# Kernel tuning notes

Hardware: AMD Instinct MI355X
Metric: run time of the kernel (lower is better)

The kernel has to match this reference:

```python
import jax, jax.numpy as jnp
import numpy as np

B, T, C = 2, 2048, 2048
N_HEAD, N_KV = 16, 4
HD = C // N_HEAD          # 128
ROPE_THETA = 10000.0


def setup_inputs() -> dict:
    key = jax.random.key(0)
    ks = jax.random.split(key, 6)
    std = 0.02
    x = jax.random.normal(ks[0], (B, T, C), dtype=jnp.float32)
    Wq = jax.random.normal(ks[1], (C, C), dtype=jnp.float32) * std
    Wk = jax.random.normal(ks[2], (C, N_KV * HD), dtype=jnp.float32) * std
    Wv = jax.random.normal(ks[3], (C, N_KV * HD), dtype=jnp.float32) * std
    Wo = jax.random.normal(ks[4], (C, C), dtype=jnp.float32) * std
    # real RoPE frequencies: freqs_cis = exp(i * t * theta^{-2j/hd})
    inv_freq = 1.0 / (ROPE_THETA ** (jnp.arange(0, HD, 2, dtype=jnp.float32) / HD))
    ang = jnp.arange(T, dtype=jnp.float32)[:, None] * inv_freq[None, :]  # [T, HD//2]
    return {"x": x, "Wq": Wq, "Wk": Wk, "Wv": Wv, "Wo": Wo,
            "freqs_cos": jnp.cos(ang), "freqs_sin": jnp.sin(ang)}


def _rope(t, cos, sin):
    # t: [B, H, T, HD]; cos/sin: [T, HD//2] -> complex rotate even/odd pairs
    tr = t.reshape(*t.shape[:-1], HD // 2, 2)
    re, im = tr[..., 0], tr[..., 1]
    c = cos[None, None, :, :]
    s = sin[None, None, :, :]
    out = jnp.stack([re * c - im * s, re * s + im * c], axis=-1)
    return out.reshape(t.shape)


def reference(x, Wq, Wk, Wv, Wo, freqs_cos, freqs_sin):
    Bm, Tm, Cm = x.shape
    q = (x @ Wq).reshape(Bm, Tm, N_HEAD, HD).transpose(0, 2, 1, 3)  # [B,H,T,HD]
    k = (x @ Wk).reshape(Bm, Tm, N_KV, HD).transpose(0, 2, 1, 3)    # [B,Hkv,T,HD]
    v = (x @ Wv).reshape(Bm, Tm, N_KV, HD).transpose(0, 2, 1, 3)
    q = _rope(q, freqs_cos, freqs_sin)
    k = _rope(k, freqs_cos, freqs_sin)
    rep = N_HEAD // N_KV
    k = jnp.repeat(k, rep, axis=1)  # GQA repeat_kv -> [B,H,T,HD]
    v = jnp.repeat(v, rep, axis=1)
    scale = 1.0 / jnp.sqrt(jnp.asarray(HD, dtype=x.dtype))
    att = jnp.einsum("bhqd,bhkd->bhqk", q, k) * scale
    causal = jnp.tril(jnp.ones((Tm, Tm), dtype=bool))
    att = jnp.where(causal[None, None], att, jnp.asarray(-jnp.inf, att.dtype))
    att = jax.nn.softmax(att, axis=-1)
    y = jnp.einsum("bhqk,bhkd->bhqd", att, v)
    y = y.transpose(0, 2, 1, 3).reshape(Bm, Tm, Cm)
    return y @ Wo
```

## Files before the change

### kernel.cpp

```cpp
#include <hip/hip_runtime.h>

#define B_ 2
#define T_ 2048
#define C_ 2048
#define NH_ 16
#define NKV_ 4
#define HD_ 128
#define REP_ (NH_ / NKV_)
#define LDQKV 3072

typedef unsigned short u16;
typedef __bf16 bf16x8v __attribute__((ext_vector_type(8)));
typedef float f32x4v __attribute__((ext_vector_type(4)));

__device__ __forceinline__ u16 f2bf(float f) {
    unsigned int u;
    __builtin_memcpy(&u, &f, 4);
    u += 0x7FFFu + ((u >> 16) & 1u);
    return (u16)(u >> 16);
}
__device__ __forceinline__ unsigned int pk2(float a, float b) {
    unsigned int ua, ub;
    __builtin_memcpy(&ua, &a, 4);
    __builtin_memcpy(&ub, &b, 4);
    ua += 0x8000u; ub += 0x8000u;
    return (ua >> 16) | (ub & 0xFFFF0000u);
}
__device__ __forceinline__ bf16x8v load8(const u16* p) {
    return *reinterpret_cast<const bf16x8v*>(p);
}
__device__ __forceinline__ void gl16(const u16* g, u16* l) {
    __builtin_amdgcn_global_load_lds(
        (const __attribute__((address_space(1))) void*)(g),
        (__attribute__((address_space(3))) void*)(l), 16, 0, 0);
}

__global__ void cvt_f32_bf16(const float* __restrict__ in, u16* __restrict__ out, int n4) {
    int i = blockIdx.x * blockDim.x + threadIdx.x;
    if (i >= n4) return;
    float4 v = reinterpret_cast<const float4*>(in)[i];
    ushort4 o;
    o.x = f2bf(v.x); o.y = f2bf(v.y); o.z = f2bf(v.z); o.w = f2bf(v.w);
    reinterpret_cast<ushort4*>(out)[i] = o;
}

__global__ void xpose_f32_bf16(const float* __restrict__ in, u16* __restrict__ out,
                               int R, int Cc) {
    __shared__ u16 tile[32][33];
    int bx = blockIdx.x * 32, by = blockIdx.y * 32;
    int tx = threadIdx.x, ty = threadIdx.y;
    for (int i = 0; i < 32; i += 8)
        tile[ty + i][tx] = f2bf(in[(size_t)(by + ty + i) * Cc + bx + tx]);
    __syncthreads();
    for (int i = 0; i < 32; i += 8)
        out[(size_t)(bx + ty + i) * R + by + tx] = tile[tx][ty + i];
}

__global__ __launch_bounds__(256) void gemm_qkv(const u16* __restrict__ A,
                                                const u16* __restrict__ BT,
                                                u16* __restrict__ Cq,
                                                u16* __restrict__ vtb,
                                                int M, int N, int K) {
    __shared__ __align__(16) u16 As[128 * 32];
    __shared__ __align__(16) u16 Bs[128 * 32];
    int tid = threadIdx.x;
    int lane = tid & 63, wave = tid >> 6;
    int wm = wave & 1, wn = wave >> 1;
    int row = lane & 15, quad = lane >> 4;
    int m0 = blockIdx.y * 128, n0 = blockIdx.x * 128;

    int r_ = tid >> 2, c_ = tid & 3;
    int gch = c_ ^ ((r_ >> 1) & 3);
    const u16* gA = A + (size_t)(m0 + r_) * K + gch * 8;
    const u16* gB = BT + (size_t)(n0 + r_) * K + gch * 8;
    u16* lA = As + tid * 8;
    u16* lB = Bs + tid * 8;

    int swf = (quad ^ ((row >> 1) & 3)) * 8;
    const u16* a0 = As + (wm * 64 + row) * 32 + swf;
    const u16* b0 = Bs + (wn * 64 + row) * 32 + swf;

    f32x4v acc[4][4] = {};
    for (int k0 = 0; k0 < K; k0 += 32) {
        __syncthreads();
        gl16(gA, lA); gl16(gA + (size_t)64 * K, lA + 2048);
        gl16(gB, lB); gl16(gB + (size_t)64 * K, lB + 2048);
        gA += 32; gB += 32;
        __syncthreads();
        bf16x8v af[4], bfv[4];
        for (int t = 0; t < 4; t++) {
            af[t] = load8(a0 + t * 512);
            bfv[t] = load8(b0 + t * 512);
        }
        for (int mt = 0; mt < 4; mt++)
            for (int nt = 0; nt < 4; nt++)
                acc[mt][nt] = __builtin_amdgcn_mfma_f32_16x16x32_bf16(
                    af[mt], bfv[nt], acc[mt][nt], 0, 0, 0);
    }

    if (n0 >= 2560) {
        for (int mt = 0; mt < 4; mt++)
            for (int nt = 0; nt < 4; nt++) {
                int hd = n0 + wn * 64 + nt * 16 + row - 2560;
                int mbase = m0 + wm * 64 + mt * 16 + quad * 4;
                int bb = mbase >> 11, tok = mbase & 2047;
                int g = (tok & 31) >> 2;
                int off = (tok & ~31) + ((g & 3) * 8 + (g >> 2) * 4);
                ushort4 pk;
                pk.x = f2bf(acc[mt][nt][0]);
                pk.y = f2bf(acc[mt][nt][1]);
                pk.z = f2bf(acc[mt][nt][2]);
                pk.w = f2bf(acc[mt][nt][3]);
                *reinterpret_cast<ushort4*>(vtb + ((size_t)bb * 512 + hd) * T_ + off) = pk;
            }
    } else {
        for (int mt = 0; mt < 4; mt++)
            for (int nt = 0; nt < 4; nt++) {
                int c = n0 + wn * 64 + nt * 16 + row;
                for (int r = 0; r < 4; r++) {
                    int mrow = m0 + wm * 64 + mt * 16 + quad * 4 + r;
                    Cq[(size_t)mrow * N + c] = f2bf(acc[mt][nt][r]);
                }
            }
    }
}

__global__ __launch_bounds__(256) void gemm_out(const u16* __restrict__ A,
                                                const u16* __restrict__ BT,
                                                float* __restrict__ C,
                                                int M, int N, int K) {
    __shared__ __align__(16) u16 As[128 * 32];
    __shared__ __align__(16) u16 Bs[128 * 32];
    int tid = threadIdx.x;
    int lane = tid & 63, wave = tid >> 6;
    int wm = wave & 1, wn = wave >> 1;
    int row = lane & 15, quad = lane >> 4;
    int m0 = blockIdx.y * 128, n0 = blockIdx.x * 128;

    int r_ = tid >> 2, c_ = tid & 3;
    int gch = c_ ^ ((r_ >> 1) & 3);
    const u16* gA = A + (size_t)(m0 + r_) * K + gch * 8;
    const u16* gB = BT + (size_t)(n0 + r_) * K + gch * 8;
    u16* lA = As + tid * 8;
    u16* lB = Bs + tid * 8;

    int swf = (quad ^ ((row >> 1) & 3)) * 8;
    const u16* a0 = As + (wm * 64 + row) * 32 + swf;
    const u16* b0 = Bs + (wn * 64 + row) * 32 + swf;

    f32x4v acc[4][4] = {};
    for (int k0 = 0; k0 < K; k0 += 32) {
        __syncthreads();
        gl16(gA, lA); gl16(gA + (size_t)64 * K, lA + 2048);
        gl16(gB, lB); gl16(gB + (size_t)64 * K, lB + 2048);
        gA += 32; gB += 32;
        __syncthreads();
        bf16x8v af[4], bfv[4];
        for (int t = 0; t < 4; t++) {
            af[t] = load8(a0 + t * 512);
            bfv[t] = load8(b0 + t * 512);
        }
        for (int mt = 0; mt < 4; mt++)
            for (int nt = 0; nt < 4; nt++)
                acc[mt][nt] = __builtin_amdgcn_mfma_f32_16x16x32_bf16(
                    af[mt], bfv[nt], acc[mt][nt], 0, 0, 0);
    }

    for (int mt = 0; mt < 4; mt++)
        for (int nt = 0; nt < 4; nt++) {
            int c = n0 + wn * 64 + nt * 16 + row;
            for (int r = 0; r < 4; r++) {
                int mrow = m0 + wm * 64 + mt * 16 + quad * 4 + r;
                C[(size_t)mrow * N + c] = acc[mt][nt][r];
            }
        }
}

__global__ void rope_fused(u16* __restrict__ qkvb, const float* __restrict__ cb,
                           const float* __restrict__ sb, int totq) {
    int idx = blockIdx.x * blockDim.x + threadIdx.x;
    int nheads, off;
    if (idx < totq) { nheads = NH_; off = 0; }
    else { idx -= totq; nheads = NKV_; off = 2048; }
    int i = idx & 63;
    int h = (idx >> 6) % nheads;
    int bt = idx / (64 * nheads);
    int tt = bt & (T_ - 1);
    u16* p = qkvb + (size_t)bt * LDQKV + off + h * HD_ + 2 * i;
    unsigned int ure = ((unsigned int)p[0]) << 16, uim = ((unsigned int)p[1]) << 16;
    float re, im;
    __builtin_memcpy(&re, &ure, 4);
    __builtin_memcpy(&im, &uim, 4);
    float c = cb[tt * 64 + i], s = sb[tt * 64 + i];
    p[0] = f2bf(re * c - im * s);
    p[1] = f2bf(re * s + im * c);
}

__device__ __forceinline__ void stage_k128(const u16* kB, u16* Kl, int kt, int tid) {
    int keyc = tid >> 4, ch = tid & 15;
    const u16* g = kB + (size_t)(kt + keyc) * LDQKV + (ch ^ keyc) * 8;
    u16* l = Kl + tid * 8;
    for (int j = 0; j < 8; j++) {
        gl16(g, l);
        g += (size_t)16 * LDQKV;
        l += 2048;
    }
}
__device__ __forceinline__ void stage_v128(const u16* vB, u16* Vl, int kt, int tid) {
    int hdc = tid >> 4, ch = tid & 15;
    const u16* g = vB + (size_t)hdc * T_ + kt + (ch ^ hdc) * 8;
    u16* l = Vl + tid * 8;
    for (int j = 0; j < 8; j++) {
        gl16(g, l);
        g += (size_t)16 * T_;
        l += 2048;
    }
}

__global__ __launch_bounds__(256) void flash_k(const u16* __restrict__ qkv,
                                               const u16* __restrict__ vtb,
                                               u16* __restrict__ yb) {
    __shared__ __align__(16) u16 Kl[128 * 128];
    __shared__ __align__(16) u16 Vl[128 * 128];
    int h = blockIdx.y, b = blockIdx.z;
    int kv = h / REP_;
    int tid = threadIdx.x;
    int lane = tid & 63, wave = tid >> 6;
    int m15 = lane & 15, quad = lane >> 4;
    const u16* kB = qkv + (size_t)b * T_ * LDQKV + 2048 + kv * HD_;
    const u16* vB = vtb + ((size_t)(b * NKV_ + kv)) * HD_ * T_;
    const float scale2 = 0.1275173723f;
    const float M0b = 8.0f;
    const float NEG = -3.0e38f;

    for (int p = 0; p < 2; p++) {
        int qt = (p == 0) ? (int)blockIdx.x : (31 - (int)blockIdx.x);
        int qt0 = qt * 64;
        int qrow = qt0 + wave * 16;
        int q_i = qrow + m15;
        const u16* qp = qkv + (size_t)(b * T_ + q_i) * LDQKV + h * HD_ + quad * 8;
        bf16x8v qf[4];
        for (int kc = 0; kc < 4; kc++) qf[kc] = load8(qp + kc * 32);
        f32x4v o[8] = {};
        f32x4v lacc = {};

        int iters = qt0 / 128 + 1;
        for (int it = 0; it < iters; it++) {
            int kt = it * 128;
            __syncthreads();
            stage_k128(kB, Kl, kt, tid);
            stage_v128(vB, Vl, kt, tid);
            __syncthreads();
            f32x4v s4[8];
            for (int nt = 0; nt < 8; nt++) s4[nt] = (f32x4v){0.f, 0.f, 0.f, 0.f};
            for (int nt = 0; nt < 8; nt++) {
                const u16* kls = Kl + (nt * 16 + m15) * 128;
                for (int kc = 0; kc < 4; kc++)
                    s4[nt] = __builtin_amdgcn_mfma_f32_16x16x32_bf16(
                        load8(kls + (((kc * 4 + quad) ^ m15) * 8)), qf[kc], s4[nt], 0, 0, 0);
            }
            if (kt + 128 > qt0) {
                for (int nt = 0; nt < 8; nt++) {
                    int key = kt + nt * 16 + quad * 4;
                    for (int r = 0; r < 4; r++)
                        if (key + r > q_i) s4[nt][r] = NEG;
                }
            }
            for (int nt = 0; nt < 8; nt++) {
                for (int r = 0; r < 4; r++)
                    s4[nt][r] = exp2f(fmaf(s4[nt][r], scale2, -M0b));
                lacc += s4[nt];
            }
            for (int c = 0; c < 4; c++) {
                unsigned int w[4];
                w[0] = pk2(s4[2 * c][0], s4[2 * c][1]);
                w[1] = pk2(s4[2 * c][2], s4[2 * c][3]);
                w[2] = pk2(s4[2 * c + 1][0], s4[2 * c + 1][1]);
                w[3] = pk2(s4[2 * c + 1][2], s4[2 * c + 1][3]);
                bf16x8v pf;
                __builtin_memcpy(&pf, w, 16);
                for (int dt = 0; dt < 8; dt++) {
                    const u16* vls = Vl + (dt * 16 + m15) * 128;
                    o[dt] = __builtin_amdgcn_mfma_f32_16x16x32_bf16(
                        load8(vls + (((c * 4 + quad) ^ m15) * 8)), pf, o[dt], 0, 0, 0);
                }
            }
        }
        float l = lacc[0] + lacc[1] + lacc[2] + lacc[3];
        l += __shfl_xor(l, 16, 64);
        l += __shfl_xor(l, 32, 64);
        float inv = 1.f / l;
        u16* yp = yb + (size_t)(b * T_ + q_i) * C_ + h * HD_ + quad * 4;
        for (int dt = 0; dt < 8; dt++) {
            ushort4 pk;
            pk.x = f2bf(o[dt][0] * inv);
            pk.y = f2bf(o[dt][1] * inv);
            pk.z = f2bf(o[dt][2] * inv);
            pk.w = f2bf(o[dt][3] * inv);
            *reinterpret_cast<ushort4*>(yp + dt * 16) = pk;
        }
    }
}

extern "C" void kernel_launch(void* const* d_in, const int* in_sizes, int n_in,
                              void* d_out, int out_size, void* d_ws, size_t ws_size,
                              hipStream_t stream) {
    const float* x  = (const float*)d_in[0];
    const float* Wq = (const float*)d_in[1];
    const float* Wk = (const float*)d_in[2];
    const float* Wv = (const float*)d_in[3];
    const float* Wo = (const float*)d_in[4];
    const float* fc = (const float*)d_in[5];
    const float* fs = (const float*)d_in[6];
    float* out = (float*)d_out;

    char* ws = (char*)d_ws;
    u16* WqkvT = (u16*)(ws);
    u16* WoT   = (u16*)(ws + 12582912);
    u16* xb    = (u16*)(ws + 20971520);
    u16* qkvb  = (u16*)(ws + 37748736);
    u16* vtb   = (u16*)(ws + 62914560);
    u16* yb    = (u16*)(ws + 67108864);

    const int M = B_ * T_;

    int n4 = (M * C_) / 4;
    cvt_f32_bf16<<<n4 / 256, 256, 0, stream>>>(x, xb, n4);

    dim3 tb(32, 8);
    xpose_f32_bf16<<<dim3(C_ / 32, C_ / 32), tb, 0, stream>>>(Wq, WqkvT, C_, C_);
    xpose_f32_bf16<<<dim3((NKV_ * HD_) / 32, C_ / 32), tb, 0, stream>>>(Wk, WqkvT + 2048 * 2048, C_, NKV_ * HD_);
    xpose_f32_bf16<<<dim3((NKV_ * HD_) / 32, C_ / 32), tb, 0, stream>>>(Wv, WqkvT + 2560 * 2048, C_, NKV_ * HD_);
    xpose_f32_bf16<<<dim3(C_ / 32, C_ / 32), tb, 0, stream>>>(Wo, WoT, C_, C_);

    gemm_qkv<<<dim3(LDQKV / 128, M / 128), 256, 0, stream>>>(xb, WqkvT, qkvb, vtb, M, LDQKV, C_);

    int totq = M * NH_ * (HD_ / 2);
    int totk = M * NKV_ * (HD_ / 2);
    rope_fused<<<(totq + totk) / 256, 256, 0, stream>>>(qkvb, fc, fs, totq);

    flash_k<<<dim3(T_ / 128, NH_, B_), 256, 0, stream>>>(qkvb, vtb, yb);

    gemm_out<<<dim3(C_ / 128, M / 128), 256, 0, stream>>>(yb, WoT, out, M, C_, C_);
}
```

Before: 324.9 us.

## Fuse RoPE into QKV GEMM epilogue and deepen GEMM K-tile to 64

Removes the separate RoPE kernel by applying the rotation in the QKV GEMM epilogue, using a lane shuffle to fetch the even/odd partner value. This saves a full read-modify-write pass over the Q/K buffer and one kernel launch. Both GEMMs also stage a 64-wide K slice per iteration with a new 8-way XOR swizzle, halving the number of barrier pairs per K step. In exchange, LDS use per block doubles and the epilogue does more scattered loads of the cos/sin tables.

After: 314.3 us. 1.03x faster.

```diff
diff --git a/kernel.cpp b/kernel.cpp
--- a/kernel.cpp
+++ b/kernel.cpp
@@ -60,48 +60,55 @@
                                                 const u16* __restrict__ BT,
                                                 u16* __restrict__ Cq,
                                                 u16* __restrict__ vtb,
+                                                const float* __restrict__ cb,
+                                                const float* __restrict__ sb,
                                                 int M, int N, int K) {
-    __shared__ __align__(16) u16 As[128 * 32];
-    __shared__ __align__(16) u16 Bs[128 * 32];
+    __shared__ __align__(16) u16 As[128 * 64];
+    __shared__ __align__(16) u16 Bs[128 * 64];
     int tid = threadIdx.x;
     int lane = tid & 63, wave = tid >> 6;
     int wm = wave & 1, wn = wave >> 1;
-    int row = lane & 15, quad = lane >> 4;
+    int m15 = lane & 15, quad = lane >> 4;
     int m0 = blockIdx.y * 128, n0 = blockIdx.x * 128;
 
-    int r_ = tid >> 2, c_ = tid & 3;
-    int gch = c_ ^ ((r_ >> 1) & 3);
+    int r_ = tid >> 3, c_ = tid & 7;
+    int gch = c_ ^ (r_ & 7);
     const u16* gA = A + (size_t)(m0 + r_) * K + gch * 8;
     const u16* gB = BT + (size_t)(n0 + r_) * K + gch * 8;
     u16* lA = As + tid * 8;
     u16* lB = Bs + tid * 8;
 
-    int swf = (quad ^ ((row >> 1) & 3)) * 8;
-    const u16* a0 = As + (wm * 64 + row) * 32 + swf;
-    const u16* b0 = Bs + (wn * 64 + row) * 32 + swf;
+    int sw8 = m15 & 7;
+    const u16* a0 = As + (wm * 64 + m15) * 64;
+    const u16* b0 = Bs + (wn * 64 + m15) * 64;
 
     f32x4v acc[4][4] = {};
-    for (int k0 = 0; k0 < K; k0 += 32) {
+    for (int k0 = 0; k0 < K; k0 += 64) {
         __syncthreads();
-        gl16(gA, lA); gl16(gA + (size_t)64 * K, lA + 2048);
-        gl16(gB, lB); gl16(gB + (size_t)64 * K, lB + 2048);
-        gA += 32; gB += 32;
+        for (int j = 0; j < 4; j++) {
+            gl16(gA + (size_t)(32 * j) * K, lA + j * 2048);
+            gl16(gB + (size_t)(32 * j) * K, lB + j * 2048);
+        }
+        gA += 64; gB += 64;
         __syncthreads();
-        bf16x8v af[4], bfv[4];
-        for (int t = 0; t < 4; t++) {
-            af[t] = load8(a0 + t * 512);
-            bfv[t] = load8(b0 + t * 512);
-        }
-        for (int mt = 0; mt < 4; mt++)
-            for (int nt = 0; nt < 4; nt++)
-                acc[mt][nt] = __builtin_amdgcn_mfma_f32_16x16x32_bf16(
-                    af[mt], bfv[nt], acc[mt][nt], 0, 0, 0);
+        for (int kc = 0; kc < 2; kc++) {
+            int co = ((kc * 4 + quad) ^ sw8) * 8;
+            bf16x8v af[4], bfv[4];
+            for (int t = 0; t < 4; t++) {
+                af[t] = load8(a0 + t * 1024 + co);
+                bfv[t] = load8(b0 + t * 1024 + co);
+            }
+            for (int mt = 0; mt < 4; mt++)
+                for (int nt = 0; nt < 4; nt++)
+                    acc[mt][nt] = __builtin_amdgcn_mfma_f32_16x16x32_bf16(
+                        af[mt], bfv[nt], acc[mt][nt], 0, 0, 0);
+        }
     }
 
     if (n0 >= 2560) {
         for (int mt = 0; mt < 4; mt++)
             for (int nt = 0; nt < 4; nt++) {
-                int hd = n0 + wn * 64 + nt * 16 + row - 2560;
+                int hd = n0 + wn * 64 + nt * 16 + m15 - 2560;
                 int mbase = m0 + wm * 64 + mt * 16 + quad * 4;
                 int bb = mbase >> 11, tok = mbase & 2047;
                 int g = (tok & 31) >> 2;
@@ -116,10 +123,18 @@
     } else {
         for (int mt = 0; mt < 4; mt++)
             for (int nt = 0; nt < 4; nt++) {
-                int c = n0 + wn * 64 + nt * 16 + row;
+                int c = n0 + wn * 64 + nt * 16 + m15;
+                int i = (c & 127) >> 1;
+                float sgn = (c & 1) ? 1.f : -1.f;
                 for (int r = 0; r < 4; r++) {
                     int mrow = m0 + wm * 64 + mt * 16 + quad * 4 + r;
-                    Cq[(size_t)mrow * N + c] = f2bf(acc[mt][nt][r]);
+                    int tok = mrow & 2047;
+                    float cv = cb[tok * 64 + i];
+                    float sv = sb[tok * 64 + i];
+                    float v = acc[mt][nt][r];
+                    float pval = __shfl_xor(v, 1, 64);
+                    float outv = fmaf(v, cv, pval * sv * sgn);
+                    Cq[(size_t)mrow * N + c] = f2bf(outv);
                 }
             }
     }
@@ -129,71 +144,56 @@
                                                 const u16* __restrict__ BT,
                                                 float* __restrict__ C,
                                                 int M, int N, int K) {
-    __shared__ __align__(16) u16 As[128 * 32];
-    __shared__ __align__(16) u16 Bs[128 * 32];
+    __shared__ __align__(16) u16 As[128 * 64];
+    __shared__ __align__(16) u16 Bs[128 * 64];
     int tid = threadIdx.x;
     int lane = tid & 63, wave = tid >> 6;
     int wm = wave & 1, wn = wave >> 1;
-    int row = lane & 15, quad = lane >> 4;
+    int m15 = lane & 15, quad = lane >> 4;
     int m0 = blockIdx.y * 128, n0 = blockIdx.x * 128;
 
-    int r_ = tid >> 2, c_ = tid & 3;
-    int gch = c_ ^ ((r_ >> 1) & 3);
+    int r_ = tid >> 3, c_ = tid & 7;
+    int gch = c_ ^ (r_ & 7);
     const u16* gA = A + (size_t)(m0 + r_) * K + gch * 8;
     const u16* gB = BT + (size_t)(n0 + r_) * K + gch * 8;
     u16* lA = As + tid * 8;
     u16* lB = Bs + tid * 8;
 
-    int swf = (quad ^ ((row >> 1) & 3)) * 8;
-    const u16* a0 = As + (wm * 64 + row) * 32 + swf;
-    const u16* b0 = Bs + (wn * 64 + row) * 32 + swf;
+    int sw8 = m15 & 7;
+    const u16* a0 = As + (wm * 64 + m15) * 64;
+    const u16* b0 = Bs + (wn * 64 + m15) * 64;
 
     f32x4v acc[4][4] = {};
-    for (int k0 = 0; k0 < K; k0 += 32) {
+    for (int k0 = 0; k0 < K; k0 += 64) {
         __syncthreads();
-        gl16(gA, lA); gl16(gA + (size_t)64 * K, lA + 2048);
-        gl16(gB, lB); gl16(gB + (size_t)64 * K, lB + 2048);
-        gA += 32; gB += 32;
+        for (int j = 0; j < 4; j++) {
+            gl16(gA + (size_t)(32 * j) * K, lA + j * 2048);
+            gl16(gB + (size_t)(32 * j) * K, lB + j * 2048);
+        }
+        gA += 64; gB += 64;
         __syncthreads();
-        bf16x8v af[4], bfv[4];
-        for (int t = 0; t < 4; t++) {
-            af[t] = load8(a0 + t * 512);
-            bfv[t] = load8(b0 + t * 512);
-        }
-        for (int mt = 0; mt < 4; mt++)
-            for (int nt = 0; nt < 4; nt++)
-                acc[mt][nt] = __builtin_amdgcn_mfma_f32_16x16x32_bf16(
-                    af[mt], bfv[nt], acc[mt][nt], 0, 0, 0);
+        for (int kc = 0; kc < 2; kc++) {
+            int co = ((kc * 4 + quad) ^ sw8) * 8;
+            bf16x8v af[4], bfv[4];
+            for (int t = 0; t < 4; t++) {
+                af[t] = load8(a0 + t * 1024 + co);
+                bfv[t] = load8(b0 + t * 1024 + co);
+            }
+            for (int mt = 0; mt < 4; mt++)
+                for (int nt = 0; nt < 4; nt++)
+                    acc[mt][nt] = __builtin_amdgcn_mfma_f32_16x16x32_bf16(
+                        af[mt], bfv[nt], acc[mt][nt], 0, 0, 0);
+        }
     }
 
     for (int mt = 0; mt < 4; mt++)
         for (int nt = 0; nt < 4; nt++) {
-            int c = n0 + wn * 64 + nt * 16 + row;
+            int c = n0 + wn * 64 + nt * 16 + m15;
             for (int r = 0; r < 4; r++) {
                 int mrow = m0 + wm * 64 + mt * 16 + quad * 4 + r;
                 C[(size_t)mrow * N + c] = acc[mt][nt][r];
             }
         }
-}
-
-__global__ void rope_fused(u16* __restrict__ qkvb, const float* __restrict__ cb,
-                           const float* __restrict__ sb, int totq) {
-    int idx = blockIdx.x * blockDim.x + threadIdx.x;
-    int nheads, off;
-    if (idx < totq) { nheads = NH_; off = 0; }
-    else { idx -= totq; nheads = NKV_; off = 2048; }
-    int i = idx & 63;
-    int h = (idx >> 6) % nheads;
-    int bt = idx / (64 * nheads);
-    int tt = bt & (T_ - 1);
-    u16* p = qkvb + (size_t)bt * LDQKV + off + h * HD_ + 2 * i;
-    unsigned int ure = ((unsigned int)p[0]) << 16, uim = ((unsigned int)p[1]) << 16;
-    float re, im;
-    __builtin_memcpy(&re, &ure, 4);
-    __builtin_memcpy(&im, &uim, 4);
-    float c = cb[tt * 64 + i], s = sb[tt * 64 + i];
-    p[0] = f2bf(re * c - im * s);
-    p[1] = f2bf(re * s + im * c);
 }
 
 __device__ __forceinline__ void stage_k128(const u16* kB, u16* Kl, int kt, int tid) {
@@ -333,11 +333,7 @@
     xpose_f32_bf16<<<dim3((NKV_ * HD_) / 32, C_ / 32), tb, 0, stream>>>(Wv, WqkvT + 2560 * 2048, C_, NKV_ * HD_);
     xpose_f32_bf16<<<dim3(C_ / 32, C_ / 32), tb, 0, stream>>>(Wo, WoT, C_, C_);
 
-    gemm_qkv<<<dim3(LDQKV / 128, M / 128), 256, 0, stream>>>(xb, WqkvT, qkvb, vtb, M, LDQKV, C_);
-
-    int totq = M * NH_ * (HD_ / 2);
-    int totk = M * NKV_ * (HD_ / 2);
-    rope_fused<<<(totq + totk) / 256, 256, 0, stream>>>(qkvb, fc, fs, totq);
+    gemm_qkv<<<dim3(LDQKV / 128, M / 128), 256, 0, stream>>>(xb, WqkvT, qkvb, vtb, fc, fs, M, LDQKV, C_);
 
     flash_k<<<dim3(T_ / 128, NH_, B_), 256, 0, stream>>>(qkvb, vtb, yb);
 
```

## Fuse RoPE into QKV GEMM epilogue and merge prep kernels into one launch

Applied to the files above, without the earlier changes.

Applies rotary embedding directly in the QKV GEMM epilogue, using a lane shuffle to fetch the paired even/odd element. This removes the separate RoPE kernel and its extra read-modify-write pass over the Q/K buffer. The bf16 cast of x and the four weight transposes are also combined into a single prep launch with block-range dispatch, cutting launch overhead. The tradeoff is extra per-element cos/sin global loads in the GEMM epilogue.

New measurement: 336.7 us. +3.7%, slower.

```diff
diff --git a/kernel.cpp b/kernel.cpp
--- a/kernel.cpp
+++ b/kernel.cpp
@@ -35,20 +35,13 @@
         (__attribute__((address_space(3))) void*)(l), 16, 0, 0);
 }
 
-__global__ void cvt_f32_bf16(const float* __restrict__ in, u16* __restrict__ out, int n4) {
-    int i = blockIdx.x * blockDim.x + threadIdx.x;
-    if (i >= n4) return;
-    float4 v = reinterpret_cast<const float4*>(in)[i];
-    ushort4 o;
-    o.x = f2bf(v.x); o.y = f2bf(v.y); o.z = f2bf(v.z); o.w = f2bf(v.w);
-    reinterpret_cast<ushort4*>(out)[i] = o;
-}
-
-__global__ void xpose_f32_bf16(const float* __restrict__ in, u16* __restrict__ out,
-                               int R, int Cc) {
+__device__ __forceinline__ void xpose_job(const float* __restrict__ in,
+                                          u16* __restrict__ out,
+                                          int R, int Cc, int local, int tid) {
     __shared__ u16 tile[32][33];
-    int bx = blockIdx.x * 32, by = blockIdx.y * 32;
-    int tx = threadIdx.x, ty = threadIdx.y;
+    int nbx = Cc / 32;
+    int bx = (local % nbx) * 32, by = (local / nbx) * 32;
+    int tx = tid & 31, ty = tid >> 5;
     for (int i = 0; i < 32; i += 8)
         tile[ty + i][tx] = f2bf(in[(size_t)(by + ty + i) * Cc + bx + tx]);
     __syncthreads();
@@ -56,17 +49,45 @@
         out[(size_t)(bx + ty + i) * R + by + tx] = tile[tx][ty + i];
 }
 
+__global__ __launch_bounds__(256) void prep(const float* __restrict__ x,
+                                            const float* __restrict__ Wq,
+                                            const float* __restrict__ Wk,
+                                            const float* __restrict__ Wv,
+                                            const float* __restrict__ Wo,
+                                            u16* __restrict__ xb,
+                                            u16* __restrict__ WqkvT,
+                                            u16* __restrict__ WoT) {
+    int blk = blockIdx.x, tid = threadIdx.x;
+    if (blk < 8192) {
+        int i = blk * 256 + tid;
+        float4 v = reinterpret_cast<const float4*>(x)[i];
+        ushort4 o;
+        o.x = f2bf(v.x); o.y = f2bf(v.y); o.z = f2bf(v.z); o.w = f2bf(v.w);
+        reinterpret_cast<ushort4*>(xb)[i] = o;
+    } else if (blk < 12288) {
+        xpose_job(Wq, WqkvT, C_, C_, blk - 8192, tid);
+    } else if (blk < 13312) {
+        xpose_job(Wk, WqkvT + 2048 * 2048, C_, NKV_ * HD_, blk - 12288, tid);
+    } else if (blk < 14336) {
+        xpose_job(Wv, WqkvT + 2560 * 2048, C_, NKV_ * HD_, blk - 13312, tid);
+    } else {
+        xpose_job(Wo, WoT, C_, C_, blk - 14336, tid);
+    }
+}
+
 __global__ __launch_bounds__(256) void gemm_qkv(const u16* __restrict__ A,
                                                 const u16* __restrict__ BT,
                                                 u16* __restrict__ Cq,
                                                 u16* __restrict__ vtb,
+                                                const float* __restrict__ cb,
+                                                const float* __restrict__ sb,
                                                 int M, int N, int K) {
     __shared__ __align__(16) u16 As[128 * 32];
     __shared__ __align__(16) u16 Bs[128 * 32];
     int tid = threadIdx.x;
     int lane = tid & 63, wave = tid >> 6;
     int wm = wave & 1, wn = wave >> 1;
-    int row = lane & 15, quad = lane >> 4;
+    int m15 = lane & 15, quad = lane >> 4;
     int m0 = blockIdx.y * 128, n0 = blockIdx.x * 128;
 
     int r_ = tid >> 2, c_ = tid & 3;
@@ -76,9 +97,9 @@
     u16* lA = As + tid * 8;
     u16* lB = Bs + tid * 8;
 
-    int swf = (quad ^ ((row >> 1) & 3)) * 8;
-    const u16* a0 = As + (wm * 64 + row) * 32 + swf;
-    const u16* b0 = Bs + (wn * 64 + row) * 32 + swf;
+    int swf = (quad ^ ((m15 >> 1) & 3)) * 8;
+    const u16* a0 = As + (wm * 64 + m15) * 32 + swf;
+    const u16* b0 = Bs + (wn * 64 + m15) * 32 + swf;
 
     f32x4v acc[4][4] = {};
     for (int k0 = 0; k0 < K; k0 += 32) {
@@ -101,7 +122,7 @@
     if (n0 >= 2560) {
         for (int mt = 0; mt < 4; mt++)
             for (int nt = 0; nt < 4; nt++) {
-                int hd = n0 + wn * 64 + nt * 16 + row - 2560;
+                int hd = n0 + wn * 64 + nt * 16 + m15 - 2560;
                 int mbase = m0 + wm * 64 + mt * 16 + quad * 4;
                 int bb = mbase >> 11, tok = mbase & 2047;
                 int g = (tok & 31) >> 2;
@@ -116,10 +137,18 @@
     } else {
         for (int mt = 0; mt < 4; mt++)
             for (int nt = 0; nt < 4; nt++) {
-                int c = n0 + wn * 64 + nt * 16 + row;
+                int c = n0 + wn * 64 + nt * 16 + m15;
+                int i = (c & 127) >> 1;
+                float sgn = (c & 1) ? 1.f : -1.f;
                 for (int r = 0; r < 4; r++) {
                     int mrow = m0 + wm * 64 + mt * 16 + quad * 4 + r;
-                    Cq[(size_t)mrow * N + c] = f2bf(acc[mt][nt][r]);
+                    int tok = mrow & 2047;
+                    float cv = cb[tok * 64 + i];
+                    float sv = sb[tok * 64 + i];
+                    float v = acc[mt][nt][r];
+                    float pval = __shfl_xor(v, 1, 64);
+                    float outv = fmaf(v, cv, pval * sv * sgn);
+                    Cq[(size_t)mrow * N + c] = f2bf(outv);
                 }
             }
     }
@@ -134,7 +163,7 @@
     int tid = threadIdx.x;
     int lane = tid & 63, wave = tid >> 6;
     int wm = wave & 1, wn = wave >> 1;
-    int row = lane & 15, quad = lane >> 4;
+    int m15 = lane & 15, quad = lane >> 4;
     int m0 = blockIdx.y * 128, n0 = blockIdx.x * 128;
 
     int r_ = tid >> 2, c_ = tid & 3;
@@ -144,9 +173,9 @@
     u16* lA = As + tid * 8;
     u16* lB = Bs + tid * 8;
 
-    int swf = (quad ^ ((row >> 1) & 3)) * 8;
-    const u16* a0 = As + (wm * 64 + row) * 32 + swf;
-    const u16* b0 = Bs + (wn * 64 + row) * 32 + swf;
+    int swf = (quad ^ ((m15 >> 1) & 3)) * 8;
+    const u16* a0 = As + (wm * 64 + m15) * 32 + swf;
+    const u16* b0 = Bs + (wn * 64 + m15) * 32 + swf;
 
     f32x4v acc[4][4] = {};
     for (int k0 = 0; k0 < K; k0 += 32) {
@@ -168,32 +197,12 @@
 
     for (int mt = 0; mt < 4; mt++)
         for (int nt = 0; nt < 4; nt++) {
-            int c = n0 + wn * 64 + nt * 16 + row;
+            int c = n0 + wn * 64 + nt * 16 + m15;
             for (int r = 0; r < 4; r++) {
                 int mrow = m0 + wm * 64 + mt * 16 + quad * 4 + r;
                 C[(size_t)mrow * N + c] = acc[mt][nt][r];
             }
         }
-}
-
-__global__ void rope_fused(u16* __restrict__ qkvb, const float* __restrict__ cb,
-                           const float* __restrict__ sb, int totq) {
-    int idx = blockIdx.x * blockDim.x + threadIdx.x;
-    int nheads, off;
-    if (idx < totq) { nheads = NH_; off = 0; }
-    else { idx -= totq; nheads = NKV_; off = 2048; }
-    int i = idx & 63;
-    int h = (idx >> 6) % nheads;
-    int bt = idx / (64 * nheads);
-    int tt = bt & (T_ - 1);
-    u16* p = qkvb + (size_t)bt * LDQKV + off + h * HD_ + 2 * i;
-    unsigned int ure = ((unsigned int)p[0]) << 16, uim = ((unsigned int)p[1]) << 16;
-    float re, im;
-    __builtin_memcpy(&re, &ure, 4);
-    __builtin_memcpy(&im, &uim, 4);
-    float c = cb[tt * 64 + i], s = sb[tt * 64 + i];
-    p[0] = f2bf(re * c - im * s);
-    p[1] = f2bf(re * s + im * c);
 }
 
 __device__ __forceinline__ void stage_k128(const u16* kB, u16* Kl, int kt, int tid) {
@@ -324,20 +333,9 @@
 
     const int M = B_ * T_;
 
-    int n4 = (M * C_) / 4;
-    cvt_f32_bf16<<<n4 / 256, 256, 0, stream>>>(x, xb, n4);
-
-    dim3 tb(32, 8);
-    xpose_f32_bf16<<<dim3(C_ / 32, C_ / 32), tb, 0, stream>>>(Wq, WqkvT, C_, C_);
-    xpose_f32_bf16<<<dim3((NKV_ * HD_) / 32, C_ / 32), tb, 0, stream>>>(Wk, WqkvT + 2048 * 2048, C_, NKV_ * HD_);
-    xpose_f32_bf16<<<dim3((NKV_ * HD_) / 32, C_ / 32), tb, 0, stream>>>(Wv, WqkvT + 2560 * 2048, C_, NKV_ * HD_);
-    xpose_f32_bf16<<<dim3(C_ / 32, C_ / 32), tb, 0, stream>>>(Wo, WoT, C_, C_);
-
-    gemm_qkv<<<dim3(LDQKV / 128, M / 128), 256, 0, stream>>>(xb, WqkvT, qkvb, vtb, M, LDQKV, C_);
-
-    int totq = M * NH_ * (HD_ / 2);
-    int totk = M * NKV_ * (HD_ / 2);
-    rope_fused<<<(totq + totk) / 256, 256, 0, stream>>>(qkvb, fc, fs, totq);
+    prep<<<18432, 256, 0, stream>>>(x, Wq, Wk, Wv, Wo, xb, WqkvT, WoT);
+
+    gemm_qkv<<<dim3(LDQKV / 128, M / 128), 256, 0, stream>>>(xb, WqkvT, qkvb, vtb, fc, fs, M, LDQKV, C_);
 
     flash_k<<<dim3(T_ / 128, NH_, B_), 256, 0, stream>>>(qkvb, vtb, yb);
 
```
